# Performance work log

Measured on AMD Instinct MI355X. Metric: run time of the kernel, lower is better.

Reference implementation:

```python
import jax, jax.numpy as jnp
import numpy as np

B, S, NK, H, D, DM = 2, 2048, 32, 8, 64, 512
NEG = -1e9


def setup_inputs() -> dict:
    key = jax.random.key(0)
    ks = jax.random.split(key, 12)
    hidden_states = jax.random.normal(ks[0], (B, S, DM), jnp.float32)
    rpe = jax.random.normal(ks[1], (B, S, NK, H), jnp.float32)
    idx = jax.random.randint(ks[2], (S, NK), 0, S)
    pad = jax.random.uniform(ks[3], (S, NK)) < 0.1
    q_k_mask = jnp.where(pad, -1, idx).astype(jnp.int32)
    k_q_mask = jax.random.randint(ks[4], (S, NK), 0, S).astype(jnp.int32)  # only used by TVM backward
    sc = 0.02
    w_q = jax.random.normal(ks[5], (DM, H * D), jnp.float32) * sc
    w_k = jax.random.normal(ks[6], (DM, H * D), jnp.float32) * sc
    w_v = jax.random.normal(ks[7], (DM, H * D), jnp.float32) * sc
    fc_w = jax.random.normal(ks[8], (H * D, DM), jnp.float32) * sc
    fc_b = jnp.zeros((DM,), jnp.float32)
    ln_g = jnp.ones((DM,), jnp.float32)
    ln_b = jnp.zeros((DM,), jnp.float32)
    return {"hidden_states": hidden_states, "rpe": rpe, "q_k_mask": q_k_mask,
            "k_q_mask": k_q_mask, "w_q": w_q, "w_k": w_k, "w_v": w_v,
            "fc_w": fc_w, "fc_b": fc_b, "ln_g": ln_g, "ln_b": ln_b}


def reference(hidden_states, rpe, q_k_mask, k_q_mask, w_q, w_k, w_v, fc_w, fc_b, ln_g, ln_b):
    bsz, seq_len, _ = hidden_states.shape
    q = (hidden_states @ w_q).reshape(bsz, seq_len, H, D)
    k = (hidden_states @ w_k).reshape(bsz, seq_len, H, D)
    v = (hidden_states @ w_v).reshape(bsz, seq_len, H, D)

    valid = q_k_mask >= 0                      # [S, NK]
    idx = jnp.where(valid, q_k_mask, 0)        # safe gather index
    vmask = valid[None, :, None, :]            # [1,S,1,NK] broadcast over (b, h)

    # QKP_mm_tvm: sparse QK^T over neighbor lists, plus relative-position bias,
    # padded slots -> -1e9.  k_g: [B,S,NK,H,D]
    k_g = k[:, idx]
    scores = jnp.einsum('bshd,bsnhd->bshn', q, k_g) + rpe.transpose(0, 1, 3, 2)
    scores = jnp.where(vmask, scores, NEG)
    scores = scores / (D ** 0.5)

    attn = jax.nn.softmax(scores, axis=-1)
    # AttnV_mm_tvm with padding 0: padded slots contribute nothing.
    attn = attn * vmask
    v_g = v[:, idx]                            # [B,S,NK,H,D]
    ctx = jnp.einsum('bshn,bsnhd->bshd', attn, v_g).reshape(bsz, seq_len, H * D)

    out = ctx @ fc_w + fc_b + hidden_states    # dropout = identity (eval)
    mu = jnp.mean(out, axis=-1, keepdims=True)
    var = jnp.mean((out - mu) ** 2, axis=-1, keepdims=True)
    return (out - mu) * jax.lax.rsqrt(var + 1e-6) * ln_g + ln_b
```

## Files before the change

### kernel.cpp

```cpp
#include <hip/hip_runtime.h>
#include <hip/hip_bf16.h>

constexpr int Bb  = 2;
constexpr int Ss  = 2048;
constexpr int NKk = 32;
constexpr int Hh  = 8;
constexpr int DMm = 512;
constexpr int Mm  = Bb * Ss;
constexpr int QKV = 1536;

typedef __attribute__((ext_vector_type(8))) short bf16x8;
typedef __attribute__((ext_vector_type(4))) float f32x4;

__device__ __forceinline__ float b2f(unsigned short u) {
  return __uint_as_float((unsigned)u << 16);
}
__device__ __forceinline__ unsigned short f2b(float f) {
  unsigned u = __float_as_uint(f);
  unsigned r = (u + 0x7fffu + ((u >> 16) & 1u)) >> 16;
  return (unsigned short)r;
}
__device__ __forceinline__ void gload_lds16(const ushort* g, ushort* l) {
  __builtin_amdgcn_global_load_lds(
      (const __attribute__((address_space(1))) void*)g,
      (__attribute__((address_space(3))) void*)l, 16, 0, 0);
}

__global__ __launch_bounds__(256) void cvt_bf16_k(
    const float* __restrict__ x, ushort* __restrict__ y, int n8)
{
  const int i = blockIdx.x * 256 + threadIdx.x;
  if (i >= n8) return;
  const float4 a = reinterpret_cast<const float4*>(x)[2 * i];
  const float4 b = reinterpret_cast<const float4*>(x)[2 * i + 1];
  ushort o[8] = {f2b(a.x), f2b(a.y), f2b(a.z), f2b(a.w),
                 f2b(b.x), f2b(b.y), f2b(b.z), f2b(b.w)};
  reinterpret_cast<uint4*>(y)[i] = *reinterpret_cast<uint4*>(o);
}

__global__ __launch_bounds__(256) void cvt_wt_k(
    const float* __restrict__ Wq, const float* __restrict__ Wk,
    const float* __restrict__ Wv, const float* __restrict__ Wf,
    ushort* __restrict__ Wt3, ushort* __restrict__ Wtf)
{
  __shared__ float tile[64][65];
  const int z = blockIdx.z;
  const float* W = (z == 0) ? Wq : (z == 1) ? Wk : (z == 2) ? Wv : Wf;
  ushort* Wt = (z < 3) ? (Wt3 + (size_t)z * 512 * 512) : Wtf;

  const int k0 = blockIdx.x * 64, n0 = blockIdx.y * 64;
  const int t = threadIdx.x;
#pragma unroll
  for (int p = 0; p < 4; ++p) {
    const int r = (t >> 4) + p * 16, c = (t & 15) * 4;
    const float4 v = *reinterpret_cast<const float4*>(&W[(size_t)(k0 + r) * 512 + n0 + c]);
    tile[r][c] = v.x; tile[r][c + 1] = v.y; tile[r][c + 2] = v.z; tile[r][c + 3] = v.w;
  }
  __syncthreads();
  const int n = t >> 2, ks = (t & 3) * 16;
  ushort o[16];
#pragma unroll
  for (int i = 0; i < 16; ++i) o[i] = f2b(tile[ks + i][n]);
  *reinterpret_cast<uint4*>(&Wt[(size_t)(n0 + n) * 512 + k0 + ks])     = *reinterpret_cast<uint4*>(&o[0]);
  *reinterpret_cast<uint4*>(&Wt[(size_t)(n0 + n) * 512 + k0 + ks + 8]) = *reinterpret_cast<uint4*>(&o[8]);
}

template <int OUT_BF16>
__global__ __launch_bounds__(256) void gemm_mfma(
    const ushort* __restrict__ Xb, const ushort* __restrict__ Wt,
    void* __restrict__ Yv, const float* __restrict__ bias,
    const float* __restrict__ resid, int ldY)
{
  __shared__ ushort As[128][72];
  __shared__ ushort Bs[64][72];
  const int bm = blockIdx.x * 128;
  const int bn = blockIdx.y * 64;
  const int t = threadIdx.x;
  const int wave = t >> 6, lane = t & 63;
  const int wm = (wave >> 1) * 64;
  const int wn = (wave & 1) * 32;

  f32x4 acc[4][2] = {};

  for (int k0 = 0; k0 < 512; k0 += 64) {
#pragma unroll
    for (int p = 0; p < 4; ++p) {
      const int i = p * 256 + t;
      const int row = i >> 3, kc = (i & 7) * 8;
      *reinterpret_cast<uint4*>(&As[row][kc]) =
          *reinterpret_cast<const uint4*>(&Xb[(size_t)(bm + row) * 512 + k0 + kc]);
    }
#pragma unroll
    for (int p = 0; p < 2; ++p) {
      const int i = p * 256 + t;
      const int row = i >> 3, kc = (i & 7) * 8;
      *reinterpret_cast<uint4*>(&Bs[row][kc]) =
          *reinterpret_cast<const uint4*>(&Wt[(size_t)(bn + row) * 512 + k0 + kc]);
    }
    __syncthreads();
#pragma unroll
    for (int ks = 0; ks < 2; ++ks) {
      const int kk = ks * 32 + (lane >> 4) * 8;
      bf16x8 af[4], bfr[2];
#pragma unroll
      for (int i = 0; i < 4; ++i)
        af[i] = *reinterpret_cast<const bf16x8*>(&As[wm + i * 16 + (lane & 15)][kk]);
#pragma unroll
      for (int j = 0; j < 2; ++j)
        bfr[j] = *reinterpret_cast<const bf16x8*>(&Bs[wn + j * 16 + (lane & 15)][kk]);
#pragma unroll
      for (int i = 0; i < 4; ++i)
#pragma unroll
        for (int j = 0; j < 2; ++j)
          acc[i][j] = __builtin_amdgcn_mfma_f32_16x16x32_bf16(af[i], bfr[j], acc[i][j], 0, 0, 0);
    }
    __syncthreads();
  }

  if (OUT_BF16) {
#pragma unroll
    for (int i = 0; i < 4; ++i)
#pragma unroll
      for (int j = 0; j < 2; ++j)
#pragma unroll
        for (int r = 0; r < 4; ++r)
          As[wm + i * 16 + (lane >> 4) * 4 + r][wn + j * 16 + (lane & 15)] = f2b(acc[i][j][r]);
    __syncthreads();
    ushort* Y = reinterpret_cast<ushort*>(Yv);
#pragma unroll
    for (int p = 0; p < 4; ++p) {
      const int i = p * 256 + t;
      const int row = i >> 3, kc = (i & 7) * 8;
      *reinterpret_cast<uint4*>(&Y[(size_t)(bm + row) * ldY + bn + kc]) =
          *reinterpret_cast<uint4*>(&As[row][kc]);
    }
  } else {
    float* Y = reinterpret_cast<float*>(Yv);
#pragma unroll
    for (int i = 0; i < 4; ++i) {
#pragma unroll
      for (int j = 0; j < 2; ++j) {
        const int m = bm + wm + i * 16 + (lane >> 4) * 4;
        const int n = bn + wn + j * 16 + (lane & 15);
        const float bb = bias[n];
#pragma unroll
        for (int r = 0; r < 4; ++r)
          Y[(size_t)(m + r) * ldY + n] = acc[i][j][r] + bb + resid[(size_t)(m + r) * 512 + n];
      }
    }
  }
}

__global__ __launch_bounds__(256) void attn_k3(
    const ushort* __restrict__ qkv, const float* __restrict__ rpe,
    const int* __restrict__ qkm, ushort* __restrict__ ctx)
{
  __shared__ ushort Ks[32 * 512];
  __shared__ float  qs[512];

  const int bs = blockIdx.x;
  const int b  = bs >> 11;
  const int s  = bs & 2047;
  const int t  = threadIdx.x;
  const int wv = t >> 6, lane = t & 63;

  const ushort* qrow = qkv + (size_t)bs * QKV;
  qs[t]       = b2f(qrow[t]);
  qs[t + 256] = b2f(qrow[t + 256]);

#pragma unroll
  for (int r = 0; r < 8; ++r) {
    const int n = r * 4 + wv;
    int im = qkm[s * NKk + n];
    im = im < 0 ? 0 : im;
    const ushort* gsrc = qkv + (size_t)(b * Ss + im) * QKV + 512
                       + ((lane ^ (n & 7)) * 8);
    gload_lds16(gsrc, &Ks[n * 512]);
  }

  int iv = qkm[s * NKk + (lane & 31)];

  __syncthreads();

  const int h = t >> 5;
  const int n = t & 31;
  const bool valid = (iv >= 0);

  float2 a2 = make_float2(0.f, 0.f);
#pragma unroll
  for (int j = 0; j < 8; ++j) {
    const int blk = (h * 8 + j) ^ (n & 7);
    const uint4 kk = *reinterpret_cast<const uint4*>(&Ks[n * 512 + blk * 8]);
    const float* qq = &qs[h * 64 + j * 8];
    a2.x += qq[0] * __uint_as_float(kk.x << 16);
    a2.y += qq[1] * __uint_as_float(kk.x & 0xffff0000u);
    a2.x += qq[2] * __uint_as_float(kk.y << 16);
    a2.y += qq[3] * __uint_as_float(kk.y & 0xffff0000u);
    a2.x += qq[4] * __uint_as_float(kk.z << 16);
    a2.y += qq[5] * __uint_as_float(kk.z & 0xffff0000u);
    a2.x += qq[6] * __uint_as_float(kk.w << 16);
    a2.y += qq[7] * __uint_as_float(kk.w & 0xffff0000u);
  }
  float sc = a2.x + a2.y + rpe[((size_t)bs * NKk + n) * Hh + h];
  sc = valid ? sc * 0.125f : -1e30f;

  float mx = sc;
#pragma unroll
  for (int m = 16; m >= 1; m >>= 1) mx = fmaxf(mx, __shfl_xor(mx, m, 32));
  const float p = valid ? __expf(sc - mx) : 0.f;
  float sum = p;
#pragma unroll
  for (int m = 16; m >= 1; m >>= 1) sum += __shfl_xor(sum, m, 32);
  const float pn = (sum > 0.f) ? (p / sum) : 0.f;

  const ushort* vbase = qkv + (size_t)b * Ss * QKV + 1024;
  const int e = 2 * t;
  float c0 = 0.f, c1 = 0.f;
#pragma unroll
  for (int n2 = 0; n2 < 32; ++n2) {
    const int src = (lane & 32) + n2;
    const float a = __shfl(pn, src, 64);
    int row = __shfl(iv, src, 64);
    row = row < 0 ? 0 : row;
    const uint vvu = *reinterpret_cast<const uint*>(
        &vbase[(size_t)row * QKV + (e & 511)]);
    c0 += a * __uint_as_float(vvu << 16);
    c1 += a * __uint_as_float(vvu & 0xffff0000u);
  }
  const uint packed = (uint)f2b(c0) | ((uint)f2b(c1) << 16);
  *reinterpret_cast<uint*>(&ctx[(size_t)bs * 512 + e]) = packed;
}

__global__ __launch_bounds__(256) void ln_k(
    float* __restrict__ x, const float* __restrict__ g,
    const float* __restrict__ bta)
{
  const int w    = threadIdx.x >> 6;
  const int lane = threadIdx.x & 63;
  const int row  = blockIdx.x * 4 + w;

  float4* xr = reinterpret_cast<float4*>(x + (size_t)row * 512);
  const float4 v0 = xr[lane];
  const float4 v1 = xr[lane + 64];

  float sum = v0.x + v0.y + v0.z + v0.w + v1.x + v1.y + v1.z + v1.w;
  float sq  = v0.x * v0.x + v0.y * v0.y + v0.z * v0.z + v0.w * v0.w
            + v1.x * v1.x + v1.y * v1.y + v1.z * v1.z + v1.w * v1.w;
#pragma unroll
  for (int m = 32; m >= 1; m >>= 1) {
    sum += __shfl_xor(sum, m, 64);
    sq  += __shfl_xor(sq,  m, 64);
  }
  const float mu  = sum * (1.f / 512.f);
  const float var = sq * (1.f / 512.f) - mu * mu;
  const float rs  = rsqrtf(var + 1e-6f);

  const float4 g0 = reinterpret_cast<const float4*>(g)[lane];
  const float4 g1 = reinterpret_cast<const float4*>(g)[lane + 64];
  const float4 b0 = reinterpret_cast<const float4*>(bta)[lane];
  const float4 b1 = reinterpret_cast<const float4*>(bta)[lane + 64];

  float4 o0, o1;
  o0.x = (v0.x - mu) * rs * g0.x + b0.x;
  o0.y = (v0.y - mu) * rs * g0.y + b0.y;
  o0.z = (v0.z - mu) * rs * g0.z + b0.z;
  o0.w = (v0.w - mu) * rs * g0.w + b0.w;
  o1.x = (v1.x - mu) * rs * g1.x + b1.x;
  o1.y = (v1.y - mu) * rs * g1.y + b1.y;
  o1.z = (v1.z - mu) * rs * g1.z + b1.z;
  o1.w = (v1.w - mu) * rs * g1.w + b1.w;
  xr[lane]      = o0;
  xr[lane + 64] = o1;
}

extern "C" void kernel_launch(void* const* d_in, const int* in_sizes, int n_in,
                              void* d_out, int out_size, void* d_ws, size_t ws_size,
                              hipStream_t stream) {
  const float* hs  = (const float*)d_in[0];
  const float* rpe = (const float*)d_in[1];
  const int*   qkm = (const int*)d_in[2];
  const float* wq  = (const float*)d_in[4];
  const float* wk  = (const float*)d_in[5];
  const float* wv  = (const float*)d_in[6];
  const float* fcw = (const float*)d_in[7];
  const float* fcb = (const float*)d_in[8];
  const float* lng = (const float*)d_in[9];
  const float* lnb = (const float*)d_in[10];
  float* out = (float*)d_out;

  ushort* Xb  = (ushort*)d_ws;
  ushort* Wt3 = Xb  + (size_t)Mm * DMm;
  ushort* Wtf = Wt3 + (size_t)3 * DMm * DMm;
  ushort* qkv = Wtf + (size_t)DMm * DMm;
  ushort* cxb = qkv + (size_t)Mm * QKV;

  cvt_bf16_k<<<(Mm * DMm / 8 + 255) / 256, 256, 0, stream>>>(hs, Xb, Mm * DMm / 8);
  cvt_wt_k<<<dim3(8, 8, 4), 256, 0, stream>>>(wq, wk, wv, fcw, Wt3, Wtf);

  gemm_mfma<1><<<dim3(Mm / 128, QKV / 64), 256, 0, stream>>>(
      Xb, Wt3, qkv, nullptr, nullptr, QKV);

  attn_k3<<<Mm, 256, 0, stream>>>(qkv, rpe, qkm, cxb);

  gemm_mfma<0><<<dim3(Mm / 128, DMm / 64), 256, 0, stream>>>(
      cxb, Wtf, out, fcb, hs, DMm);
  ln_k<<<Mm / 4, 256, 0, stream>>>(out, lng, lnb);
}
```

Before: 64.44 us.

## Use direct global-to-LDS loads with XOR swizzle and wider QKV GEMM tile

The GEMM kernel now stages A and B tiles with global_load_lds straight into LDS instead of going through registers. The LDS layout is XOR-swizzled in place of the padded layout, to avoid bank conflicts on the MFMA fragment reads. The N tile becomes a template parameter, and the QKV projection uses 128-wide tiles for more reuse per block, which halves the grid and raises register use. Correctness depends on the lane-to-LDS address mapping of the direct-load instruction matching the swizzle.

```diff
diff --git a/kernel.cpp b/kernel.cpp
--- a/kernel.cpp
+++ b/kernel.cpp
@@ -65,53 +65,61 @@
   *reinterpret_cast<uint4*>(&Wt[(size_t)(n0 + n) * 512 + k0 + ks + 8]) = *reinterpret_cast<uint4*>(&o[8]);
 }
 
-template <int OUT_BF16>
-__global__ __launch_bounds__(256) void gemm_mfma(
+template <int OUT_BF16, int BNv>
+__global__ __launch_bounds__(256) void gemm_mfma2(
     const ushort* __restrict__ Xb, const ushort* __restrict__ Wt,
     void* __restrict__ Yv, const float* __restrict__ bias,
     const float* __restrict__ resid, int ldY)
 {
-  __shared__ ushort As[128][72];
-  __shared__ ushort Bs[64][72];
+  constexpr int NJ = BNv / 32;
+  constexpr int SMSZ = 8192 + BNv * 64;
+  __shared__ ushort smem[SMSZ];
+  ushort* As = smem;
+  ushort* Bs = smem + 8192;
+
   const int bm = blockIdx.x * 128;
-  const int bn = blockIdx.y * 64;
-  const int t = threadIdx.x;
+  const int bn = blockIdx.y * BNv;
+  const int t  = threadIdx.x;
   const int wave = t >> 6, lane = t & 63;
   const int wm = (wave >> 1) * 64;
-  const int wn = (wave & 1) * 32;
-
-  f32x4 acc[4][2] = {};
+  const int wn = (wave & 1) * (BNv / 2);
+
+  f32x4 acc[4][NJ] = {};
 
   for (int k0 = 0; k0 < 512; k0 += 64) {
 #pragma unroll
     for (int p = 0; p < 4; ++p) {
       const int i = p * 256 + t;
-      const int row = i >> 3, kc = (i & 7) * 8;
-      *reinterpret_cast<uint4*>(&As[row][kc]) =
-          *reinterpret_cast<const uint4*>(&Xb[(size_t)(bm + row) * 512 + k0 + kc]);
-    }
-#pragma unroll
-    for (int p = 0; p < 2; ++p) {
+      const int row = i >> 3, sb = i & 7;
+      const ushort* g = Xb + (size_t)(bm + row) * 512 + k0 + ((sb ^ (row & 7)) << 3);
+      gload_lds16(g, &As[(size_t)(p * 256 + wave * 64) * 8]);
+    }
+#pragma unroll
+    for (int p = 0; p < NJ; ++p) {
       const int i = p * 256 + t;
-      const int row = i >> 3, kc = (i & 7) * 8;
-      *reinterpret_cast<uint4*>(&Bs[row][kc]) =
-          *reinterpret_cast<const uint4*>(&Wt[(size_t)(bn + row) * 512 + k0 + kc]);
+      const int row = i >> 3, sb = i & 7;
+      const ushort* g = Wt + (size_t)(bn + row) * 512 + k0 + ((sb ^ (row & 7)) << 3);
+      gload_lds16(g, &Bs[(size_t)(p * 256 + wave * 64) * 8]);
     }
     __syncthreads();
 #pragma unroll
     for (int ks = 0; ks < 2; ++ks) {
-      const int kk = ks * 32 + (lane >> 4) * 8;
-      bf16x8 af[4], bfr[2];
+      const int kb = ks * 4 + (lane >> 4);
+      bf16x8 af[4], bfr[NJ];
+#pragma unroll
+      for (int i = 0; i < 4; ++i) {
+        const int row = wm + i * 16 + (lane & 15);
+        af[i] = *reinterpret_cast<const bf16x8*>(&As[row * 64 + ((kb ^ (row & 7)) << 3)]);
+      }
+#pragma unroll
+      for (int j = 0; j < NJ; ++j) {
+        const int row = wn + j * 16 + (lane & 15);
+        bfr[j] = *reinterpret_cast<const bf16x8*>(&Bs[row * 64 + ((kb ^ (row & 7)) << 3)]);
+      }
 #pragma unroll
       for (int i = 0; i < 4; ++i)
-        af[i] = *reinterpret_cast<const bf16x8*>(&As[wm + i * 16 + (lane & 15)][kk]);
-#pragma unroll
-      for (int j = 0; j < 2; ++j)
-        bfr[j] = *reinterpret_cast<const bf16x8*>(&Bs[wn + j * 16 + (lane & 15)][kk]);
-#pragma unroll
-      for (int i = 0; i < 4; ++i)
-#pragma unroll
-        for (int j = 0; j < 2; ++j)
+#pragma unroll
+        for (int j = 0; j < NJ; ++j)
           acc[i][j] = __builtin_amdgcn_mfma_f32_16x16x32_bf16(af[i], bfr[j], acc[i][j], 0, 0, 0);
     }
     __syncthreads();
@@ -121,25 +129,30 @@
 #pragma unroll
     for (int i = 0; i < 4; ++i)
 #pragma unroll
-      for (int j = 0; j < 2; ++j)
-#pragma unroll
-        for (int r = 0; r < 4; ++r)
-          As[wm + i * 16 + (lane >> 4) * 4 + r][wn + j * 16 + (lane & 15)] = f2b(acc[i][j][r]);
+      for (int j = 0; j < NJ; ++j)
+#pragma unroll
+        for (int r = 0; r < 4; ++r) {
+          const int row = wm + i * 16 + (lane >> 4) * 4 + r;
+          const int col = wn + j * 16 + (lane & 15);
+          smem[row * BNv + col] = f2b(acc[i][j][r]);
+        }
     __syncthreads();
     ushort* Y = reinterpret_cast<ushort*>(Yv);
-#pragma unroll
-    for (int p = 0; p < 4; ++p) {
-      const int i = p * 256 + t;
-      const int row = i >> 3, kc = (i & 7) * 8;
-      *reinterpret_cast<uint4*>(&Y[(size_t)(bm + row) * ldY + bn + kc]) =
-          *reinterpret_cast<uint4*>(&As[row][kc]);
+    constexpr int CPT = 128 * BNv / 8 / 256;
+#pragma unroll
+    for (int p = 0; p < CPT; ++p) {
+      const int c = p * 256 + t;
+      const int row = c / (BNv / 8);
+      const int cb  = c % (BNv / 8);
+      *reinterpret_cast<uint4*>(&Y[(size_t)(bm + row) * ldY + bn + cb * 8]) =
+          *reinterpret_cast<uint4*>(&smem[row * BNv + cb * 8]);
     }
   } else {
     float* Y = reinterpret_cast<float*>(Yv);
 #pragma unroll
     for (int i = 0; i < 4; ++i) {
 #pragma unroll
-      for (int j = 0; j < 2; ++j) {
+      for (int j = 0; j < NJ; ++j) {
         const int m = bm + wm + i * 16 + (lane >> 4) * 4;
         const int n = bn + wn + j * 16 + (lane & 15);
         const float bb = bias[n];
@@ -297,12 +310,12 @@
   cvt_bf16_k<<<(Mm * DMm / 8 + 255) / 256, 256, 0, stream>>>(hs, Xb, Mm * DMm / 8);
   cvt_wt_k<<<dim3(8, 8, 4), 256, 0, stream>>>(wq, wk, wv, fcw, Wt3, Wtf);
 
-  gemm_mfma<1><<<dim3(Mm / 128, QKV / 64), 256, 0, stream>>>(
+  gemm_mfma2<1, 128><<<dim3(Mm / 128, QKV / 128), 256, 0, stream>>>(
       Xb, Wt3, qkv, nullptr, nullptr, QKV);
 
   attn_k3<<<Mm, 256, 0, stream>>>(qkv, rpe, qkm, cxb);
 
-  gemm_mfma<0><<<dim3(Mm / 128, DMm / 64), 256, 0, stream>>>(
+  gemm_mfma2<0, 64><<<dim3(Mm / 128, DMm / 64), 256, 0, stream>>>(
       cxb, Wtf, out, fcb, hs, DMm);
   ln_k<<<Mm / 4, 256, 0, stream>>>(out, lng, lnb);
 }
```

Measured after the change: 63.57 us. About the same (-1.3%).
